# Kernel tuning notes

Hardware: AMD Instinct MI355X
Metric: run time of the kernel (lower is better)

## Reference

```python
import jax, jax.numpy as jnp
import numpy as np

D_MODEL = 2048
N_Q_HEADS = 32
N_KV_HEADS = 8
HEAD_DIM = D_MODEL // N_Q_HEADS  # 64
KV_DIM = HEAD_DIM * N_KV_HEADS   # 512
B, S = 2, 2048


def setup_inputs() -> dict:
    key = jax.random.key(0)
    ks = jax.random.split(key, 11)
    sc_d = 1.0 / np.sqrt(D_MODEL)
    return {
        "query": jax.random.normal(ks[0], (B, S, D_MODEL), jnp.float32),
        "key":   jax.random.normal(ks[1], (B, S, D_MODEL), jnp.float32),
        "value": jax.random.normal(ks[2], (B, S, D_MODEL), jnp.float32),
        "Wq": jax.random.normal(ks[3], (D_MODEL, D_MODEL), jnp.float32) * sc_d,
        "bq": jnp.zeros((D_MODEL,), jnp.float32),
        "Wk": jax.random.normal(ks[4], (D_MODEL, KV_DIM), jnp.float32) * sc_d,
        "bk": jnp.zeros((KV_DIM,), jnp.float32),
        "Wv": jax.random.normal(ks[5], (D_MODEL, KV_DIM), jnp.float32) * sc_d,
        "bv": jnp.zeros((KV_DIM,), jnp.float32),
        "Wo": jax.random.normal(ks[6], (D_MODEL, D_MODEL), jnp.float32) * sc_d,
        "bo": jnp.zeros((D_MODEL,), jnp.float32),
    }


def reference(query, key, value, Wq, bq, Wk, bk, Wv, bv, Wo, bo):
    b, s, _ = query.shape
    g = N_Q_HEADS // N_KV_HEADS  # num groups
    # projections
    Q = query @ Wq + bq                      # [b, s, d_model]
    K = key @ Wk + bk                        # [b, s, kv_dim]
    V = value @ Wv + bv                      # [b, s, kv_dim]
    # split heads. Torch code splits Q into groups of num_kv_heads heads,
    # and each group broadcasts per-head against the Hkv KV heads, i.e.
    # query head (grp*Hkv + j) attends against kv head j.
    Q = Q.reshape(b, s, g, N_KV_HEADS, HEAD_DIM)  # [b, s, g, hkv, d]
    K = K.reshape(b, s, N_KV_HEADS, HEAD_DIM)     # [b, s, hkv, d]
    V = V.reshape(b, s, N_KV_HEADS, HEAD_DIM)
    scale = 1.0 / jnp.sqrt(jnp.float32(HEAD_DIM))
    scores = jnp.einsum('bsghd,bthd->bghst', Q, K) * scale  # [b,g,hkv,s,s]
    attn = jax.nn.softmax(scores, axis=-1)
    out = jnp.einsum('bghst,bthd->bsghd', attn, V)          # [b,s,g,hkv,d]
    # concat over groups then heads == original head order (g major, hkv minor)
    out = out.reshape(b, s, D_MODEL)
    return out @ Wo + bo
```

## Files before the change

### kernel.cpp

```cpp
#include <hip/hip_runtime.h>
#include <cstdint>

typedef _Float16 half4 __attribute__((ext_vector_type(4)));
typedef _Float16 half8 __attribute__((ext_vector_type(8)));
typedef _Float16 half16 __attribute__((ext_vector_type(16)));
typedef float f32x4 __attribute__((ext_vector_type(4)));
typedef float f32x16 __attribute__((ext_vector_type(16)));

#define L2E 1.44269504088896340736f

__device__ __forceinline__ void gl16(const void* g, void* l) {
  __builtin_amdgcn_global_load_lds(
      (const __attribute__((address_space(1))) void*)g,
      (__attribute__((address_space(3))) void*)l, 16, 0, 0);
}

__device__ __forceinline__ uint32_t pk2(float a, float b) {
  return __builtin_bit_cast(uint32_t, __builtin_amdgcn_cvt_pkrtz(a, b));
}

__device__ __forceinline__ void plswap(uint32_t& x, uint32_t& y) {
  auto r = __builtin_amdgcn_permlane32_swap((int)x, (int)y, false, false);
  x = (uint32_t)r[0];
  y = (uint32_t)r[1];
}

__device__ __forceinline__ f32x16 zero16() {
  f32x16 z;
  #pragma unroll
  for (int r = 0; r < 16; ++r) z[r] = 0.0f;
  return z;
}

__global__ __launch_bounds__(256) void transpose_w_all(
    const float* __restrict__ Wq, const float* __restrict__ Wk,
    const float* __restrict__ Wv, const float* __restrict__ Wo,
    _Float16* __restrict__ WqkvT, _Float16* __restrict__ WoT)
{
  int id = blockIdx.x;
  const float* src;
  _Float16* dst;
  int N, tx, ty;
  if (id < 4096)      { src = Wq; dst = WqkvT;                        N = 2048; tx = id & 63; ty = id >> 6; }
  else if (id < 5120) { id -= 4096; src = Wk; dst = WqkvT + (size_t)2048 * 2048; N = 512; tx = id & 15; ty = id >> 4; }
  else if (id < 6144) { id -= 5120; src = Wv; dst = WqkvT + (size_t)2560 * 2048; N = 512; tx = id & 15; ty = id >> 4; }
  else                { id -= 6144; src = Wo; dst = WoT;              N = 2048; tx = id & 63; ty = id >> 6; }
  const int n0 = tx * 32, k0 = ty * 32;
  __shared__ float t[32][33];
  #pragma unroll
  for (int i = 0; i < 4; ++i)
    t[threadIdx.y + i * 8][threadIdx.x] =
        src[(size_t)(k0 + threadIdx.y + i * 8) * N + n0 + threadIdx.x];
  __syncthreads();
  #pragma unroll
  for (int i = 0; i < 4; ++i)
    dst[(size_t)(n0 + threadIdx.y + i * 8) * 2048 + k0 + threadIdx.x] =
        (_Float16)t[threadIdx.x][threadIdx.y + i * 8];
}

__global__ __launch_bounds__(256) void transpose_v(
    const _Float16* __restrict__ QKV, _Float16* __restrict__ VT)
{
  const int bh = blockIdx.z;
  const int bb = bh >> 3, h = bh & 7;
  const int t0 = blockIdx.x * 32, d0 = blockIdx.y * 32;
  __shared__ _Float16 t[32][33];
  const _Float16* src = QKV + (size_t)(bb * 2048) * 3072 + 2560 + h * 64;
  #pragma unroll
  for (int i = 0; i < 4; ++i)
    t[threadIdx.y + i * 8][threadIdx.x] =
        src[(size_t)(t0 + threadIdx.y + i * 8) * 3072 + d0 + threadIdx.x];
  __syncthreads();
  _Float16* dst = VT + ((size_t)(bb * 8 + h) * 64) * 2048;
  #pragma unroll
  for (int i = 0; i < 4; ++i)
    dst[(size_t)(d0 + threadIdx.y + i * 8) * 2048 + t0 + threadIdx.x] =
        t[threadIdx.x][threadIdx.y + i * 8];
}

template<int MODE>
__global__ __launch_bounds__(512, 1) void gemm256(
    const float* __restrict__ Fq, const float* __restrict__ Fk, const float* __restrict__ Fv,
    const _Float16* __restrict__ Ah,
    const _Float16* __restrict__ Bt,
    const float* __restrict__ bias0, const float* __restrict__ bias1, const float* __restrict__ bias2,
    _Float16* __restrict__ Ch, float* __restrict__ Cf)
{
  constexpr int K = 2048;
  constexpr int N = (MODE == 0) ? 3072 : 2048;
  constexpr int NB = N / 256;
  constexpr int G = 16 * NB;
  constexpr int ABYTES = (MODE == 0) ? 32768 : 16384;
  constexpr int BUF = ABYTES + 16384;
  constexpr int NVM = (MODE == 0) ? 6 : 4;

  const int wg = blockIdx.x;
  const int work = (wg & 7) * (G / 8) + (wg >> 3);
  const int m0 = (work / NB) * 256;
  const int n0 = (work % NB) * 256;

  const float* Af = Fq;
  if constexpr (MODE == 0) { if (n0 >= 2560) Af = Fv; else if (n0 >= 2048) Af = Fk; }

  const int tid = threadIdx.x;
  const int lane = tid & 63;
  const int w = tid >> 6;
  const int wr = w >> 2;
  const int wc = w & 3;
  const int lo = lane & 15, hi = lane >> 4;

  __shared__ __align__(1024) char smem[3 * BUF];

  f32x4 acc[8][4];
  #pragma unroll
  for (int mt = 0; mt < 8; ++mt)
    #pragma unroll
    for (int nt = 0; nt < 4; ++nt)
      acc[mt][nt] = (f32x4){0.f, 0.f, 0.f, 0.f};

  const _Float16* pB = Bt + (size_t)(n0 + w * 32 + (lane >> 2)) * K + (lane & 3) * 8;
  const size_t bstep = (size_t)16 * K;
  const int dstB = ABYTES + w * 2048;

  const int li = lane >> 3;
  const int kslot = (lane & 7) ^ li;
  const float* pA32 = nullptr;
  const _Float16* pA16 = nullptr;
  if constexpr (MODE == 0)
    pA32 = Af + (size_t)(m0 + w * 32 + li) * K + kslot * 4;
  else
    pA16 = Ah + (size_t)(m0 + w * 32 + (lane >> 2)) * K + (lane & 3) * 8;
  const size_t a32step = (size_t)8 * K;
  const int dstA = w * 4096;

  #define STAGE_TILE(buf)                                                     \
    do {                                                                      \
      char* bp_ = smem + (buf) * BUF;                                         \
      if constexpr (MODE == 0) {                                              \
        gl16(pA32,               bp_ + dstA);                                 \
        gl16(pA32 + a32step,     bp_ + dstA + 1024);                          \
        gl16(pA32 + 2 * a32step, bp_ + dstA + 2048);                          \
        gl16(pA32 + 3 * a32step, bp_ + dstA + 3072);                          \
      } else {                                                                \
        gl16(pA16,               bp_ + (w * 2048));                           \
        gl16(pA16 + bstep,       bp_ + (w * 2048) + 1024);                    \
      }                                                                       \
      gl16(pB,         bp_ + dstB);                                           \
      gl16(pB + bstep, bp_ + dstB + 1024);                                    \
    } while (0)

  #define ADVANCE()                                                           \
    do {                                                                      \
      if constexpr (MODE == 0) pA32 += 32; else pA16 += 32;                   \
      pB += 32;                                                               \
    } while (0)

  STAGE_TILE(0); ADVANCE();
  STAGE_TILE(1); ADVANCE();
  asm volatile("s_waitcnt vmcnt(%0)" :: "i"(NVM) : "memory");
  __builtin_amdgcn_s_barrier();

  const int sx = (lo & 7) << 4;
  const int ao0 = ((2 * hi) << 4) ^ sx;
  const int ao1 = ((2 * hi + 1) << 4) ^ sx;
  const int arow0 = wr * 128 + lo;
  const int abase16 = (wr * 128 + lo) * 64 + hi * 16;
  const int bbase = ABYTES + (wc * 64 + lo) * 64 + hi * 16;

  int c = 0;
  for (int t = 0; t < 64; ++t) {
    int c1 = c + 1; if (c1 == 3) c1 = 0;
    int c2 = c1 + 1; if (c2 == 3) c2 = 0;
    if (t < 62) { STAGE_TILE(c2); ADVANCE(); }

    const char* bc = smem + c * BUF;
    half8 af[8], bf[4];
    if constexpr (MODE == 0) {
      #pragma unroll
      for (int mt = 0; mt < 8; ++mt) {
        const char* rb = bc + (arow0 + mt * 16) * 128;
        f32x4 a0 = *(const f32x4*)(rb + ao0);
        f32x4 a1 = *(const f32x4*)(rb + ao1);
        union { uint32_t u[4]; half8 h; } cv;
        cv.u[0] = pk2(a0[0], a0[1]);
        cv.u[1] = pk2(a0[2], a0[3]);
        cv.u[2] = pk2(a1[0], a1[1]);
        cv.u[3] = pk2(a1[2], a1[3]);
        af[mt] = cv.h;
      }
    } else {
      #pragma unroll
      for (int mt = 0; mt < 8; ++mt)
        af[mt] = *(const half8*)(bc + abase16 + mt * 1024);
    }
    #pragma unroll
    for (int nt = 0; nt < 4; ++nt) bf[nt] = *(const half8*)(bc + bbase + nt * 1024);

    __builtin_amdgcn_s_setprio(1);
    #pragma unroll
    for (int mt = 0; mt < 8; ++mt)
      #pragma unroll
      for (int nt = 0; nt < 4; ++nt)
        acc[mt][nt] = __builtin_amdgcn_mfma_f32_16x16x32_f16(af[mt], bf[nt], acc[mt][nt], 0, 0, 0);
    __builtin_amdgcn_s_setprio(0);

    if (t < 62)       asm volatile("s_waitcnt vmcnt(%0)" :: "i"(NVM) : "memory");
    else if (t == 62) asm volatile("s_waitcnt vmcnt(0)" ::: "memory");
    if (t < 63) __builtin_amdgcn_s_barrier();
    c = c1;
  }
  #undef STAGE_TILE
  #undef ADVANCE

  float* T = (float*)smem;
  const int tr = tid >> 4;
  const int sc = tid & 15;
  #pragma unroll
  for (int mp = 0; mp < 8; ++mp) {
    __syncthreads();
    #pragma unroll
    for (int nt = 0; nt < 4; ++nt)
      #pragma unroll
      for (int r = 0; r < 4; ++r)
        T[(wr * 16 + 4 * hi + r) * 256 + wc * 64 + nt * 16 + lo] = acc[mp][nt][r];
    __syncthreads();
    const int grow = m0 + (tr >> 4) * 128 + mp * 16 + (tr & 15);
    const int gcol = n0 + sc * 16;
    const float* Trow = T + tr * 256 + sc * 16;
    float4 v[4];
    #pragma unroll
    for (int q = 0; q < 4; ++q) v[q] = ((const float4*)Trow)[q];
    const float* bp = bias0;
    int cb = gcol;
    if constexpr (MODE == 0) {
      if (gcol >= 2560) { bp = bias2; cb = gcol - 2560; }
      else if (gcol >= 2048) { bp = bias1; cb = gcol - 2048; }
    }
    float4 bvv[4];
    #pragma unroll
    for (int q = 0; q < 4; ++q) bvv[q] = ((const float4*)(bp + cb))[q];
    if constexpr (MODE == 0) {
      half16 o;
      #pragma unroll
      for (int q = 0; q < 4; ++q) {
        o[4 * q + 0] = (_Float16)(v[q].x + bvv[q].x);
        o[4 * q + 1] = (_Float16)(v[q].y + bvv[q].y);
        o[4 * q + 2] = (_Float16)(v[q].z + bvv[q].z);
        o[4 * q + 3] = (_Float16)(v[q].w + bvv[q].w);
      }
      *(half16*)(Ch + (size_t)grow * N + gcol) = o;
    } else {
      float* dstp = Cf + (size_t)grow * N + gcol;
      #pragma unroll
      for (int q = 0; q < 4; ++q) {
        float4 ov = {v[q].x + bvv[q].x, v[q].y + bvv[q].y, v[q].z + bvv[q].z, v[q].w + bvv[q].w};
        ((float4*)dstp)[q] = ov;
      }
    }
  }
}

__global__ __launch_bounds__(256, 5) void attn_fwd4(
    const _Float16* __restrict__ QKV, const _Float16* __restrict__ VT,
    _Float16* __restrict__ AO)
{
  const int wg = blockIdx.x;
  const int work = (wg & 7) * 128 + (wg >> 3);
  const int bh = work >> 6;
  const int b = bh >> 3, h = bh & 7;
  const int rem = work & 63;
  const int qh = (rem >> 4) * 8 + h;
  const int qt = rem & 15;

  const int tid = threadIdx.x;
  const int lane = tid & 63;
  const int w = tid >> 6;
  const int l31 = lane & 31;
  const int hi5 = lane >> 5;
  const int r7 = l31 & 7;

  __shared__ __align__(1024) char sm[2][2][8192];

  const _Float16 QSC = (_Float16)(0.125f * L2E);
  const int qrow0 = b * 2048 + qt * 128 + w * 32 + l31;
  half8 qf[4];
  {
    const _Float16* qp = QKV + (size_t)qrow0 * 3072 + qh * 64 + hi5 * 8;
    #pragma unroll
    for (int s = 0; s < 4; ++s) {
      half8 q = *(const half8*)(qp + s * 16);
      #pragma unroll
      for (int e = 0; e < 8; ++e) q[e] = q[e] * QSC;
      qf[s] = q;
    }
  }

  const int li = lane >> 3;
  const int lc = lane & 7;
  const int kslot = lc ^ li;
  const int w16li = w * 16 + li;
  const _Float16* Ksrc = QKV + ((size_t)(b * 2048 + w16li)) * 3072 + 2048 + h * 64 + kslot * 8;
  const _Float16* Vsrc = VT + ((size_t)(b * 8 + h) * 64 + w16li) * 2048 + kslot * 8;

  f32x16 oa[2];
  oa[0] = zero16();
  oa[1] = zero16();
  float lreg = 0.f;

  {
    char* kd = &sm[0][0][0] + w * 2048;
    char* vd = &sm[0][1][0] + w * 2048;
    gl16(Ksrc, kd);
    gl16(Ksrc + (size_t)8 * 3072, kd + 1024);
    gl16(Vsrc, vd);
    gl16(Vsrc + (size_t)8 * 2048, vd + 1024);
  }
  __syncthreads();

  int cur = 0;
  for (int t = 0; t < 32; ++t) {
    if (t < 31) {
      const int t0 = (t + 1) * 64;
      char* kd = &sm[cur ^ 1][0][0] + w * 2048;
      char* vd = &sm[cur ^ 1][1][0] + w * 2048;
      const _Float16* kg = Ksrc + (size_t)t0 * 3072;
      const _Float16* vg = Vsrc + t0;
      gl16(kg, kd);
      gl16(kg + (size_t)8 * 3072, kd + 1024);
      gl16(vg, vd);
      gl16(vg + (size_t)8 * 2048, vd + 1024);
    }

    const char* Kb = &sm[cur][0][0];
    const char* Vb = &sm[cur][1][0];

    uint32_t pw[4][4];
    float ps = 0.f;
    #pragma unroll
    for (int j = 0; j < 2; ++j) {
      f32x16 sa = zero16();
      const int kr = j * 32 + l31;
      __builtin_amdgcn_s_setprio(1);
      #pragma unroll
      for (int s = 0; s < 4; ++s) {
        half8 kf = *(const half8*)(Kb + kr * 128 + (((2 * s + hi5) ^ r7) << 4));
        sa = __builtin_amdgcn_mfma_f32_32x32x16_f16(kf, qf[s], sa, 0, 0, 0);
      }
      __builtin_amdgcn_s_setprio(0);
      #pragma unroll
      for (int r = 0; r < 16; ++r) {
        const float p = __builtin_amdgcn_exp2f(sa[r]);
        sa[r] = p;
        ps += p;
      }
      #pragma unroll
      for (int hf = 0; hf < 2; ++hf) {
        const int rb = hf * 8;
        uint32_t w0 = pk2(sa[rb + 0], sa[rb + 1]);
        uint32_t w1 = pk2(sa[rb + 2], sa[rb + 3]);
        uint32_t w2 = pk2(sa[rb + 4], sa[rb + 5]);
        uint32_t w3 = pk2(sa[rb + 6], sa[rb + 7]);
        plswap(w0, w2);
        plswap(w1, w3);
        const int s = 2 * j + hf;
        pw[s][0] = w0; pw[s][1] = w1; pw[s][2] = w2; pw[s][3] = w3;
      }
    }
    ps += __shfl_xor(ps, 32);
    lreg += ps;

    __builtin_amdgcn_s_setprio(1);
    #pragma unroll
    for (int s = 0; s < 4; ++s) {
      union { uint32_t u[4]; half8 h; } p0;
      #pragma unroll
      for (int u = 0; u < 4; ++u) p0.u[u] = pw[s][u];
      #pragma unroll
      for (int i = 0; i < 2; ++i) {
        const int vr = i * 32 + l31;
        half8 vf = *(const half8*)(Vb + vr * 128 + (((2 * s + hi5) ^ r7) << 4));
        oa[i] = __builtin_amdgcn_mfma_f32_32x32x16_f16(vf, p0.h, oa[i], 0, 0, 0);
      }
    }
    __builtin_amdgcn_s_setprio(0);

    __syncthreads();
    cur ^= 1;
  }

  {
    const float inv = 1.0f / lreg;
    #pragma unroll
    for (int i = 0; i < 2; ++i) {
      _Float16* dst = AO + (size_t)qrow0 * 2048 + qh * 64 + i * 32 + hi5 * 4;
      #pragma unroll
      for (int q = 0; q < 4; ++q) {
        union { uint32_t u[2]; half4 h4; } o;
        o.u[0] = pk2(oa[i][4 * q + 0] * inv, oa[i][4 * q + 1] * inv);
        o.u[1] = pk2(oa[i][4 * q + 2] * inv, oa[i][4 * q + 3] * inv);
        *(half4*)(dst + 8 * q) = o.h4;
      }
    }
  }
}

extern "C" void kernel_launch(void* const* d_in, const int* in_sizes, int n_in,
                              void* d_out, int out_size, void* d_ws, size_t ws_size,
                              hipStream_t stream) {
  const float* query = (const float*)d_in[0];
  const float* key   = (const float*)d_in[1];
  const float* value = (const float*)d_in[2];
  const float* Wq = (const float*)d_in[3];
  const float* bq = (const float*)d_in[4];
  const float* Wk = (const float*)d_in[5];
  const float* bk = (const float*)d_in[6];
  const float* Wv = (const float*)d_in[7];
  const float* bv = (const float*)d_in[8];
  const float* Wo = (const float*)d_in[9];
  const float* bo = (const float*)d_in[10];
  float* out = (float*)d_out;

  char* ws = (char*)d_ws;
  _Float16* WqkvT = (_Float16*)(ws + 50331648);
  _Float16* WoT   = (_Float16*)(ws + 62914560);
  _Float16* QKVh  = (_Float16*)(ws + 71303168);
  _Float16* VT    = (_Float16*)(ws + 96468992);
  _Float16* aoh   = (_Float16*)(ws + 100663296);

  transpose_w_all<<<10240, dim3(32, 8), 0, stream>>>(Wq, Wk, Wv, Wo, WqkvT, WoT);
  gemm256<0><<<192, 512, 0, stream>>>(query, key, value, nullptr, WqkvT,
                                      bq, bk, bv, QKVh, nullptr);
  transpose_v<<<dim3(64, 2, 16), dim3(32, 8), 0, stream>>>(QKVh, VT);
  attn_fwd4<<<1024, 256, 0, stream>>>(QKVh, VT, aoh);
  gemm256<1><<<128, 512, 0, stream>>>(nullptr, nullptr, nullptr, aoh, WoT,
                                      bo, nullptr, nullptr, nullptr, out);
}
```

Baseline: 257.3 us.

## Convert fp32 A to fp16 in registers and halve output GEMM M-tile

The QKV projection GEMM no longer stages fp32 activations into LDS through async global-to-LDS loads. It now loads them into registers, packs them to fp16, and writes half-sized tiles to LDS, which halves the A-tile LDS footprint and simplifies the inner read path. The output projection GEMM switches to a 128-row M tile with a 256-block grid and allows two blocks per CU, to improve occupancy and fill more CUs. The trade-off is register-staged loads that need extra waits and LDS writes in the loop, plus lower per-block reuse in the output GEMM.

```diff
diff --git a/kernel.cpp b/kernel.cpp
--- a/kernel.cpp
+++ b/kernel.cpp
@@ -79,7 +79,7 @@
 }
 
 template<int MODE>
-__global__ __launch_bounds__(512, 1) void gemm256(
+__global__ __launch_bounds__(512, MODE + 1) void gemm256(
     const float* __restrict__ Fq, const float* __restrict__ Fk, const float* __restrict__ Fv,
     const _Float16* __restrict__ Ah,
     const _Float16* __restrict__ Bt,
@@ -89,14 +89,15 @@
   constexpr int K = 2048;
   constexpr int N = (MODE == 0) ? 3072 : 2048;
   constexpr int NB = N / 256;
-  constexpr int G = 16 * NB;
-  constexpr int ABYTES = (MODE == 0) ? 32768 : 16384;
+  constexpr int BM = (MODE == 0) ? 256 : 128;
+  constexpr int G = (4096 / BM) * NB;
+  constexpr int ABYTES = BM * 64;
   constexpr int BUF = ABYTES + 16384;
-  constexpr int NVM = (MODE == 0) ? 6 : 4;
+  constexpr int MT = BM / 32;
 
   const int wg = blockIdx.x;
   const int work = (wg & 7) * (G / 8) + (wg >> 3);
-  const int m0 = (work / NB) * 256;
+  const int m0 = (work / NB) * BM;
   const int n0 = (work % NB) * 256;
 
   const float* Af = Fq;
@@ -111,112 +112,137 @@
 
   __shared__ __align__(1024) char smem[3 * BUF];
 
-  f32x4 acc[8][4];
-  #pragma unroll
-  for (int mt = 0; mt < 8; ++mt)
+  f32x4 acc[MT][4];
+  #pragma unroll
+  for (int mt = 0; mt < MT; ++mt)
     #pragma unroll
     for (int nt = 0; nt < 4; ++nt)
       acc[mt][nt] = (f32x4){0.f, 0.f, 0.f, 0.f};
 
   const _Float16* pB = Bt + (size_t)(n0 + w * 32 + (lane >> 2)) * K + (lane & 3) * 8;
-  const size_t bstep = (size_t)16 * K;
   const int dstB = ABYTES + w * 2048;
 
-  const int li = lane >> 3;
-  const int kslot = (lane & 7) ^ li;
   const float* pA32 = nullptr;
   const _Float16* pA16 = nullptr;
   if constexpr (MODE == 0)
-    pA32 = Af + (size_t)(m0 + w * 32 + li) * K + kslot * 4;
+    pA32 = Af + (size_t)(m0 + w * 32 + (lane >> 2)) * K + (lane & 3) * 8;
   else
-    pA16 = Ah + (size_t)(m0 + w * 32 + (lane >> 2)) * K + (lane & 3) * 8;
-  const size_t a32step = (size_t)8 * K;
-  const int dstA = w * 4096;
-
-  #define STAGE_TILE(buf)                                                     \
-    do {                                                                      \
-      char* bp_ = smem + (buf) * BUF;                                         \
-      if constexpr (MODE == 0) {                                              \
-        gl16(pA32,               bp_ + dstA);                                 \
-        gl16(pA32 + a32step,     bp_ + dstA + 1024);                          \
-        gl16(pA32 + 2 * a32step, bp_ + dstA + 2048);                          \
-        gl16(pA32 + 3 * a32step, bp_ + dstA + 3072);                          \
-      } else {                                                                \
-        gl16(pA16,               bp_ + (w * 2048));                           \
-        gl16(pA16 + bstep,       bp_ + (w * 2048) + 1024);                    \
-      }                                                                       \
-      gl16(pB,         bp_ + dstB);                                           \
-      gl16(pB + bstep, bp_ + dstB + 1024);                                    \
-    } while (0)
-
-  #define ADVANCE()                                                           \
-    do {                                                                      \
-      if constexpr (MODE == 0) pA32 += 32; else pA16 += 32;                   \
-      pB += 32;                                                               \
-    } while (0)
-
-  STAGE_TILE(0); ADVANCE();
-  STAGE_TILE(1); ADVANCE();
-  asm volatile("s_waitcnt vmcnt(%0)" :: "i"(NVM) : "memory");
-  __builtin_amdgcn_s_barrier();
-
-  const int sx = (lo & 7) << 4;
-  const int ao0 = ((2 * hi) << 4) ^ sx;
-  const int ao1 = ((2 * hi + 1) << 4) ^ sx;
-  const int arow0 = wr * 128 + lo;
-  const int abase16 = (wr * 128 + lo) * 64 + hi * 16;
+    pA16 = Ah + (size_t)(m0 + w * 16 + (lane >> 2)) * K + (lane & 3) * 8;
+
+  if constexpr (MODE == 0) {
+    f32x4 q00 = *(const f32x4*)pA32;
+    f32x4 q01 = *(const f32x4*)(pA32 + 4);
+    f32x4 q02 = *(const f32x4*)(pA32 + (size_t)16 * K);
+    f32x4 q03 = *(const f32x4*)(pA32 + (size_t)16 * K + 4);
+    gl16(pB, smem + dstB);
+    gl16(pB + (size_t)16 * K, smem + dstB + 1024);
+    f32x4 q10 = *(const f32x4*)(pA32 + 32);
+    f32x4 q11 = *(const f32x4*)(pA32 + 36);
+    f32x4 q12 = *(const f32x4*)(pA32 + (size_t)16 * K + 32);
+    f32x4 q13 = *(const f32x4*)(pA32 + (size_t)16 * K + 36);
+    gl16(pB + 32, smem + BUF + dstB);
+    gl16(pB + 32 + (size_t)16 * K, smem + BUF + dstB + 1024);
+    pA32 += 64; pB += 64;
+    asm volatile("s_waitcnt vmcnt(0)" ::: "memory");
+    char* wp0 = smem + w * 2048 + lane * 16;
+    union { uint32_t u[4]; half8 h; } cv;
+    cv.u[0] = pk2(q00[0], q00[1]); cv.u[1] = pk2(q00[2], q00[3]);
+    cv.u[2] = pk2(q01[0], q01[1]); cv.u[3] = pk2(q01[2], q01[3]);
+    *(half8*)wp0 = cv.h;
+    cv.u[0] = pk2(q02[0], q02[1]); cv.u[1] = pk2(q02[2], q02[3]);
+    cv.u[2] = pk2(q03[0], q03[1]); cv.u[3] = pk2(q03[2], q03[3]);
+    *(half8*)(wp0 + 1024) = cv.h;
+    char* wp1 = smem + BUF + w * 2048 + lane * 16;
+    cv.u[0] = pk2(q10[0], q10[1]); cv.u[1] = pk2(q10[2], q10[3]);
+    cv.u[2] = pk2(q11[0], q11[1]); cv.u[3] = pk2(q11[2], q11[3]);
+    *(half8*)wp1 = cv.h;
+    cv.u[0] = pk2(q12[0], q12[1]); cv.u[1] = pk2(q12[2], q12[3]);
+    cv.u[2] = pk2(q13[0], q13[1]); cv.u[3] = pk2(q13[2], q13[3]);
+    *(half8*)(wp1 + 1024) = cv.h;
+    asm volatile("s_waitcnt lgkmcnt(0)" ::: "memory");
+    __builtin_amdgcn_s_barrier();
+  } else {
+    gl16(pA16, smem + w * 1024);
+    gl16(pB, smem + dstB);
+    gl16(pB + (size_t)16 * K, smem + dstB + 1024);
+    gl16(pA16 + 32, smem + BUF + w * 1024);
+    gl16(pB + 32, smem + BUF + dstB);
+    gl16(pB + 32 + (size_t)16 * K, smem + BUF + dstB + 1024);
+    pA16 += 64; pB += 64;
+    asm volatile("s_waitcnt vmcnt(3)" ::: "memory");
+    __builtin_amdgcn_s_barrier();
+  }
+
+  const int abase = (wr * (BM / 2) + lo) * 64 + hi * 16;
   const int bbase = ABYTES + (wc * 64 + lo) * 64 + hi * 16;
 
   int c = 0;
   for (int t = 0; t < 64; ++t) {
     int c1 = c + 1; if (c1 == 3) c1 = 0;
     int c2 = c1 + 1; if (c2 == 3) c2 = 0;
-    if (t < 62) { STAGE_TILE(c2); ADVANCE(); }
+    const bool st = (t < 62);
+    f32x4 ar0, ar1, ar2, ar3;
+    if (st) {
+      char* bp_ = smem + c2 * BUF;
+      if constexpr (MODE == 0) {
+        ar0 = *(const f32x4*)pA32;
+        ar1 = *(const f32x4*)(pA32 + 4);
+        ar2 = *(const f32x4*)(pA32 + (size_t)16 * K);
+        ar3 = *(const f32x4*)(pA32 + (size_t)16 * K + 4);
+        pA32 += 32;
+      } else {
+        gl16(pA16, bp_ + w * 1024);
+        pA16 += 32;
+      }
+      gl16(pB, bp_ + dstB);
+      gl16(pB + (size_t)16 * K, bp_ + dstB + 1024);
+      pB += 32;
+    }
 
     const char* bc = smem + c * BUF;
-    half8 af[8], bf[4];
-    if constexpr (MODE == 0) {
-      #pragma unroll
-      for (int mt = 0; mt < 8; ++mt) {
-        const char* rb = bc + (arow0 + mt * 16) * 128;
-        f32x4 a0 = *(const f32x4*)(rb + ao0);
-        f32x4 a1 = *(const f32x4*)(rb + ao1);
-        union { uint32_t u[4]; half8 h; } cv;
-        cv.u[0] = pk2(a0[0], a0[1]);
-        cv.u[1] = pk2(a0[2], a0[3]);
-        cv.u[2] = pk2(a1[0], a1[1]);
-        cv.u[3] = pk2(a1[2], a1[3]);
-        af[mt] = cv.h;
-      }
-    } else {
-      #pragma unroll
-      for (int mt = 0; mt < 8; ++mt)
-        af[mt] = *(const half8*)(bc + abase16 + mt * 1024);
-    }
+    half8 af[MT], bf[4];
+    #pragma unroll
+    for (int mt = 0; mt < MT; ++mt) af[mt] = *(const half8*)(bc + abase + mt * 1024);
     #pragma unroll
     for (int nt = 0; nt < 4; ++nt) bf[nt] = *(const half8*)(bc + bbase + nt * 1024);
 
     __builtin_amdgcn_s_setprio(1);
     #pragma unroll
-    for (int mt = 0; mt < 8; ++mt)
+    for (int mt = 0; mt < MT; ++mt)
       #pragma unroll
       for (int nt = 0; nt < 4; ++nt)
         acc[mt][nt] = __builtin_amdgcn_mfma_f32_16x16x32_f16(af[mt], bf[nt], acc[mt][nt], 0, 0, 0);
     __builtin_amdgcn_s_setprio(0);
 
-    if (t < 62)       asm volatile("s_waitcnt vmcnt(%0)" :: "i"(NVM) : "memory");
-    else if (t == 62) asm volatile("s_waitcnt vmcnt(0)" ::: "memory");
-    if (t < 63) __builtin_amdgcn_s_barrier();
+    if (st) {
+      if constexpr (MODE == 0) {
+        asm volatile("s_waitcnt vmcnt(2)" ::: "memory");
+        char* wp = smem + c2 * BUF + w * 2048 + lane * 16;
+        union { uint32_t u[4]; half8 h; } cv;
+        cv.u[0] = pk2(ar0[0], ar0[1]); cv.u[1] = pk2(ar0[2], ar0[3]);
+        cv.u[2] = pk2(ar1[0], ar1[1]); cv.u[3] = pk2(ar1[2], ar1[3]);
+        *(half8*)wp = cv.h;
+        cv.u[0] = pk2(ar2[0], ar2[1]); cv.u[1] = pk2(ar2[2], ar2[3]);
+        cv.u[2] = pk2(ar3[0], ar3[1]); cv.u[3] = pk2(ar3[2], ar3[3]);
+        *(half8*)(wp + 1024) = cv.h;
+      } else {
+        asm volatile("s_waitcnt vmcnt(3)" ::: "memory");
+      }
+    } else if (t == 62) {
+      asm volatile("s_waitcnt vmcnt(0)" ::: "memory");
+    }
+    if (t < 63) {
+      if constexpr (MODE == 0) asm volatile("s_waitcnt lgkmcnt(0)" ::: "memory");
+      __builtin_amdgcn_s_barrier();
+    }
     c = c1;
   }
-  #undef STAGE_TILE
-  #undef ADVANCE
 
   float* T = (float*)smem;
   const int tr = tid >> 4;
   const int sc = tid & 15;
   #pragma unroll
-  for (int mp = 0; mp < 8; ++mp) {
+  for (int mp = 0; mp < MT; ++mp) {
     __syncthreads();
     #pragma unroll
     for (int nt = 0; nt < 4; ++nt)
@@ -224,7 +250,7 @@
       for (int r = 0; r < 4; ++r)
         T[(wr * 16 + 4 * hi + r) * 256 + wc * 64 + nt * 16 + lo] = acc[mp][nt][r];
     __syncthreads();
-    const int grow = m0 + (tr >> 4) * 128 + mp * 16 + (tr & 15);
+    const int grow = m0 + (tr >> 4) * (BM / 2) + mp * 16 + (tr & 15);
     const int gcol = n0 + sc * 16;
     const float* Trow = T + tr * 256 + sc * 16;
     float4 v[4];
@@ -432,6 +458,6 @@
                                       bq, bk, bv, QKVh, nullptr);
   transpose_v<<<dim3(64, 2, 16), dim3(32, 8), 0, stream>>>(QKVh, VT);
   attn_fwd4<<<1024, 256, 0, stream>>>(QKVh, VT, aoh);
-  gemm256<1><<<128, 512, 0, stream>>>(nullptr, nullptr, nullptr, aoh, WoT,
+  gemm256<1><<<256, 512, 0, stream>>>(nullptr, nullptr, nullptr, aoh, WoT,
                                       bo, nullptr, nullptr, nullptr, out);
 }
```

After: 230.0 us. 10.6% less time.
